# Kernel tuning notes

Hardware: AMD Instinct MI355X
Metric: run time of the kernel (lower is better)

The kernel has to match this reference:

```python
import jax, jax.numpy as jnp
import numpy as np

B, D, M = 64, 256, 100  # batch, reduced channel dim, h*w of feature map (10x10)

# Precompute upper-triangle (including diagonal) flat indices for Triuvec
_r, _c = np.triu_indices(D)
FLAT_TRIU_IDX = jnp.asarray(_r * D + _c)  # [D*(D+1)/2]


def setup_inputs() -> dict:
    key = jax.random.key(0)
    k1, = jax.random.split(key, 1)
    feat_map = jax.random.normal(k1, (B, D, M), dtype=jnp.float32)
    # temperature param init: log(1 / (2 * h * w)) with h = w = 10
    temperature = jnp.full((1, 1), np.log(1.0 / (2 * 10 * 10)), dtype=jnp.float32)
    return {"feat_map": feat_map, "temperature": temperature}


def reference(feat_map, temperature):
    # feat_map: [B, D, M]; temperature: [1, 1] learned scalar
    b, d, m = feat_map.shape
    f1 = feat_map[:, :, None, :]  # [B, D, 1, M]
    f2 = feat_map[:, None, :, :]  # [B, 1, D, M]
    # item_1 - item_2, summed over map dim; idea_variant path: (i1 - i2)/2 * exp(T)
    out = 0.5 * jnp.sum(jnp.abs(f1 + f2) - jnp.abs(f1 - f2), axis=-1)  # [B, D, D]
    out = out * jnp.exp(temperature[0, 0])
    # normalize_bdc double-centering: out - (1/D) out @ 1 - (1/D) 1 @ out
    row = jnp.sum(out, axis=2, keepdims=True) / d  # [B, D, 1]
    col = jnp.sum(out, axis=1, keepdims=True) / d  # [B, 1, D]
    out = out - row - col
    # Triuvec (with diagonal): gather upper-triangle entries
    vec = out.reshape(b, d * d)[:, FLAT_TRIU_IDX]  # [B, D*(D+1)/2]
    return vec
```

## Files before the change

### kernel.cpp

```cpp
#include <hip/hip_runtime.h>


#define NB 64
#define DD 256
#define MM 100
#define TILE 64
#define NUT 10
#define TRI_PER_B 32896
#define NTILE 640
#define NM2 50
#define TILE_F (TILE * TILE)
#define PSTRIDE 192

typedef unsigned int u32;
typedef _Float16 f16x2 __attribute__((ext_vector_type(2)));
typedef _Float16 f16x4 __attribute__((ext_vector_type(4)));

__device__ __forceinline__ void tile_coords(int t, int& ti, int& tj) {
    int a = (t >= 4) + (t >= 7) + (t >= 9);
    int s = (a * (9 - a)) >> 1;
    ti = a;
    tj = t - s + a;
}

__device__ __forceinline__ u32 slot_enc(int g) {
    return g == 0 ? 0x03020100u : g == 1 ? 0x21060504u
         : g == 2 ? 0x25220807u : 0x28262309u;
}

__device__ __forceinline__ int swz_bt(int w) { return (w & 7) * 80 + (w >> 3); }

extern "C" __global__ void __launch_bounds__(256, 5)
k_partial(const float* __restrict__ f, float* __restrict__ part,
          _Float16* __restrict__ tiles) {
    __shared__ u32 As[NM2][TILE];
    __shared__ u32 Bs[NM2][32];
    const int t = threadIdx.x;
    const int unit = (blockIdx.x & 7) * 160 + (blockIdx.x >> 3);
    const int bt = unit >> 1;
    const int half = unit & 1;
    const int b = bt / NUT;
    const int ut = bt % NUT;
    int ti, tj;
    tile_coords(ut, ti, tj);
    const int i0 = ti * TILE;
    const int j0 = tj * TILE + half * 32;
    const float* fb = f + (size_t)b * DD * MM;

    for (int l = t; l < TILE * 25; l += 256) {
        const int il = l & 63;
        const int mq = l >> 6;
        float4 v = *reinterpret_cast<const float4*>(fb + (size_t)(i0 + il) * MM + mq * 4);
        As[2 * mq + 0][il] = __builtin_bit_cast(u32, __builtin_amdgcn_cvt_pkrtz(v.x, v.y));
        As[2 * mq + 1][il] = __builtin_bit_cast(u32, __builtin_amdgcn_cvt_pkrtz(v.z, v.w));
    }
    for (int l = t; l < 32 * 25; l += 256) {
        const int il = l & 31;
        const int mq = l >> 5;
        float4 w = *reinterpret_cast<const float4*>(fb + (size_t)(j0 + il) * MM + mq * 4);
        Bs[2 * mq + 0][il] = __builtin_bit_cast(u32, __builtin_amdgcn_cvt_pkrtz(w.x, w.y));
        Bs[2 * mq + 1][il] = __builtin_bit_cast(u32, __builtin_amdgcn_cvt_pkrtz(w.z, w.w));
    }
    __syncthreads();

    const int cg = t & 15;
    const int rg = t >> 4;
    float acc[4][2] = {};

    uint4 af = *reinterpret_cast<const uint4*>(&As[0][rg * 4]);
    uint2 bf = *reinterpret_cast<const uint2*>(&Bs[0][cg * 2]);
    #pragma unroll 5
    for (int m2 = 0; m2 < NM2; ++m2) {
        uint4 an;
        uint2 bn;
        if (m2 + 1 < NM2) {
            an = *reinterpret_cast<const uint4*>(&As[m2 + 1][rg * 4]);
            bn = *reinterpret_cast<const uint2*>(&Bs[m2 + 1][cg * 2]);
        }
        const u32 av[4] = {af.x, af.y, af.z, af.w};
        const u32 bv[2] = {bf.x, bf.y};
        u32 aab[4], aso[4], bab[2], bsg[2];
        #pragma unroll
        for (int q = 0; q < 4; ++q) {
            aab[q] = av[q] & 0x7fff7fffu;
            aso[q] = (av[q] & 0x80008000u) | 0x3c003c00u;
        }
        #pragma unroll
        for (int c = 0; c < 2; ++c) {
            bab[c] = bv[c] & 0x7fff7fffu;
            bsg[c] = bv[c] & 0x80008000u;
        }
        #pragma unroll
        for (int q = 0; q < 4; ++q) {
            #pragma unroll
            for (int c = 0; c < 2; ++c) {
                u32 so = aso[q] ^ bsg[c];
                f16x2 mn = __builtin_elementwise_min(
                    __builtin_bit_cast(f16x2, aab[q]),
                    __builtin_bit_cast(f16x2, bab[c]));
                acc[q][c] = __builtin_amdgcn_fdot2(
                    mn, __builtin_bit_cast(f16x2, so), acc[q][c], false);
            }
        }
        af = an; bf = bn;
    }

    _Float16* tp = tiles + (size_t)bt * TILE_F;
    #pragma unroll
    for (int q = 0; q < 4; ++q) {
        *reinterpret_cast<u32*>(tp + (rg * 4 + q) * TILE + half * 32 + cg * 2) =
            __builtin_bit_cast(u32, __builtin_amdgcn_cvt_pkrtz(acc[q][0], acc[q][1]));
    }

    float ra[4], cb[2];
    #pragma unroll
    for (int q = 0; q < 4; ++q) ra[q] = acc[q][0] + acc[q][1];
    #pragma unroll
    for (int c = 0; c < 2; ++c)
        cb[c] = (acc[0][c] + acc[1][c]) + (acc[2][c] + acc[3][c]);

    __syncthreads();
    float* red  = reinterpret_cast<float*>(&As[0][0]);
    float* red2 = red + 1024;
    #pragma unroll
    for (int q = 0; q < 4; ++q) red[cg * 64 + rg * 4 + q] = ra[q];
    #pragma unroll
    for (int c = 0; c < 2; ++c) red2[rg * 32 + cg * 2 + c] = cb[c];
    __syncthreads();

    float* pb = part + (size_t)bt * PSTRIDE;
    if (t < TILE) {
        float s = 0.f;
        #pragma unroll
        for (int w = 0; w < 16; ++w) s += red[w * 64 + t];
        pb[half * 64 + t] = s;
    } else if (t < TILE + 32 && ti != tj) {
        const int u = t - TILE;
        float s = 0.f;
        #pragma unroll
        for (int w = 0; w < 16; ++w) s += red2[w * 32 + u];
        pb[128 + half * 32 + u] = s;
    }
}

extern "C" __global__ void __launch_bounds__(256)
k_finalize(const float* __restrict__ part, const float* __restrict__ temp,
           const _Float16* __restrict__ tiles, float* __restrict__ out) {
    __shared__ float rows_sh[128];
    const int t = threadIdx.x;
    const int bt = swz_bt(blockIdx.x);
    const int b = bt / NUT;
    const int ut = bt % NUT;
    int ti, tj;
    tile_coords(ut, ti, tj);
    const int i0 = ti * TILE, j0 = tj * TILE;
    const int tix = t >> 4, tiy = t & 15;

    if (t < 128) {
        const int hr = t >> 6, u = t & 63;
        const int g = hr ? tj : ti;
        const u32 enc = slot_enc(g);
        float sum = 0.f;
        #pragma unroll
        for (int s = 0; s < 4; ++s) {
            const u32 byte = (enc >> (8 * s)) & 0xffu;
            const int ut_s = byte & 0x1f;
            const int side = byte >> 5;
            const float* pb = part + (size_t)(b * NUT + ut_s) * PSTRIDE;
            sum += side ? pb[128 + u] : (pb[u] + pb[64 + u]);
        }
        rows_sh[t] = sum;
    }

    const _Float16* tp = tiles + (size_t)bt * TILE_F;
    float acc[4][4];
    #pragma unroll
    for (int q = 0; q < 4; ++q) {
        f16x4 v = *reinterpret_cast<const f16x4*>(tp + (tix * 4 + q) * TILE + tiy * 4);
        acc[q][0] = (float)v.x; acc[q][1] = (float)v.y;
        acc[q][2] = (float)v.z; acc[q][3] = (float)v.w;
    }
    __syncthreads();

    const float scale = expf(temp[0]);
    const float inv_d = 1.0f / DD;
    const int cbase = (ti == tj) ? 0 : 64;
    float rloc[4], cloc[4];
    #pragma unroll
    for (int q = 0; q < 4; ++q) rloc[q] = rows_sh[tix * 4 + q];
    #pragma unroll
    for (int r = 0; r < 4; ++r) cloc[r] = rows_sh[cbase + tiy * 4 + r];

    float* ob = out + (size_t)b * TRI_PER_B;
    #pragma unroll
    for (int q = 0; q < 4; ++q) {
        const int i = i0 + tix * 4 + q;
        float v[4];
        #pragma unroll
        for (int r = 0; r < 4; ++r)
            v[r] = scale * (acc[q][r] - (rloc[q] + cloc[r]) * inv_d);
        const int j0e = j0 + tiy * 4;
        if (ti != tj) {
            const int off = (i * (2 * DD - i + 1)) / 2 + (j0e - i);
            *reinterpret_cast<float4*>(ob + off) = make_float4(v[0], v[1], v[2], v[3]);
        } else {
            #pragma unroll
            for (int r = 0; r < 4; ++r) {
                const int j = j0e + r;
                if (j >= i) {
                    const int off = (i * (2 * DD - i + 1)) / 2 + (j - i);
                    ob[off] = v[r];
                }
            }
        }
    }
}

extern "C" void kernel_launch(void* const* d_in, const int* in_sizes, int n_in,
                              void* d_out, int out_size, void* d_ws, size_t ws_size,
                              hipStream_t stream) {
    const float* f    = (const float*)d_in[0];
    const float* temp = (const float*)d_in[1];
    float* out  = (float*)d_out;
    float* part = (float*)d_ws;
    _Float16* tiles = (_Float16*)(part + NTILE * PSTRIDE);

    k_partial<<<2 * NTILE, 256, 0, stream>>>(f, part, tiles);
    k_finalize<<<NTILE, 256, 0, stream>>>(part, temp, tiles, out);
}
```

Measured before the change: 36.17 us.

## Interleave m-pairs in LDS, stagger chunk order, split finalize into half-tiles

```diff
diff --git a/kernel.cpp b/kernel.cpp
--- a/kernel.cpp
+++ b/kernel.cpp
@@ -8,13 +8,12 @@
 #define NUT 10
 #define TRI_PER_B 32896
 #define NTILE 640
-#define NM2 50
+#define NMQ 25
 #define TILE_F (TILE * TILE)
 #define PSTRIDE 192
 
 typedef unsigned int u32;
 typedef _Float16 f16x2 __attribute__((ext_vector_type(2)));
-typedef _Float16 f16x4 __attribute__((ext_vector_type(4)));
 
 __device__ __forceinline__ void tile_coords(int t, int& ti, int& tj) {
     int a = (t >= 4) + (t >= 7) + (t >= 9);
@@ -28,13 +27,11 @@
          : g == 2 ? 0x25220807u : 0x28262309u;
 }
 
-__device__ __forceinline__ int swz_bt(int w) { return (w & 7) * 80 + (w >> 3); }
-
 extern "C" __global__ void __launch_bounds__(256, 5)
 k_partial(const float* __restrict__ f, float* __restrict__ part,
           _Float16* __restrict__ tiles) {
-    __shared__ u32 As[NM2][TILE];
-    __shared__ u32 Bs[NM2][32];
+    __shared__ u32 As[NMQ][TILE][2];
+    __shared__ u32 Bs[NMQ][32][2];
     const int t = threadIdx.x;
     const int unit = (blockIdx.x & 7) * 160 + (blockIdx.x >> 3);
     const int bt = unit >> 1;
@@ -47,19 +44,23 @@
     const int j0 = tj * TILE + half * 32;
     const float* fb = f + (size_t)b * DD * MM;
 
-    for (int l = t; l < TILE * 25; l += 256) {
+    for (int l = t; l < TILE * NMQ; l += 256) {
         const int il = l & 63;
         const int mq = l >> 6;
         float4 v = *reinterpret_cast<const float4*>(fb + (size_t)(i0 + il) * MM + mq * 4);
-        As[2 * mq + 0][il] = __builtin_bit_cast(u32, __builtin_amdgcn_cvt_pkrtz(v.x, v.y));
-        As[2 * mq + 1][il] = __builtin_bit_cast(u32, __builtin_amdgcn_cvt_pkrtz(v.z, v.w));
-    }
-    for (int l = t; l < 32 * 25; l += 256) {
+        uint2 p;
+        p.x = __builtin_bit_cast(u32, __builtin_amdgcn_cvt_pkrtz(v.x, v.y));
+        p.y = __builtin_bit_cast(u32, __builtin_amdgcn_cvt_pkrtz(v.z, v.w));
+        *reinterpret_cast<uint2*>(&As[mq][il][0]) = p;
+    }
+    for (int l = t; l < 32 * NMQ; l += 256) {
         const int il = l & 31;
         const int mq = l >> 5;
         float4 w = *reinterpret_cast<const float4*>(fb + (size_t)(j0 + il) * MM + mq * 4);
-        Bs[2 * mq + 0][il] = __builtin_bit_cast(u32, __builtin_amdgcn_cvt_pkrtz(w.x, w.y));
-        Bs[2 * mq + 1][il] = __builtin_bit_cast(u32, __builtin_amdgcn_cvt_pkrtz(w.z, w.w));
+        uint2 p;
+        p.x = __builtin_bit_cast(u32, __builtin_amdgcn_cvt_pkrtz(w.x, w.y));
+        p.y = __builtin_bit_cast(u32, __builtin_amdgcn_cvt_pkrtz(w.z, w.w));
+        *reinterpret_cast<uint2*>(&Bs[mq][il][0]) = p;
     }
     __syncthreads();
 
@@ -67,42 +68,49 @@
     const int rg = t >> 4;
     float acc[4][2] = {};
 
-    uint4 af = *reinterpret_cast<const uint4*>(&As[0][rg * 4]);
-    uint2 bf = *reinterpret_cast<const uint2*>(&Bs[0][cg * 2]);
-    #pragma unroll 5
-    for (int m2 = 0; m2 < NM2; ++m2) {
-        uint4 an;
-        uint2 bn;
-        if (m2 + 1 < NM2) {
-            an = *reinterpret_cast<const uint4*>(&As[m2 + 1][rg * 4]);
-            bn = *reinterpret_cast<const uint2*>(&Bs[m2 + 1][cg * 2]);
-        }
-        const u32 av[4] = {af.x, af.y, af.z, af.w};
-        const u32 bv[2] = {bf.x, bf.y};
-        u32 aab[4], aso[4], bab[2], bsg[2];
-        #pragma unroll
-        for (int q = 0; q < 4; ++q) {
-            aab[q] = av[q] & 0x7fff7fffu;
-            aso[q] = (av[q] & 0x80008000u) | 0x3c003c00u;
-        }
-        #pragma unroll
-        for (int c = 0; c < 2; ++c) {
-            bab[c] = bv[c] & 0x7fff7fffu;
-            bsg[c] = bv[c] & 0x80008000u;
-        }
-        #pragma unroll
-        for (int q = 0; q < 4; ++q) {
+    const int c0 = (int)(((t >> 6) + blockIdx.x) % 5u);
+    for (int cc = 0; cc < 5; ++cc) {
+        int ch = c0 + cc;
+        if (ch >= 5) ch -= 5;
+        const int mqb = ch * 5;
+        #pragma unroll
+        for (int k = 0; k < 5; ++k) {
+            const int mq = mqb + k;
+            uint4 alo = *reinterpret_cast<const uint4*>(&As[mq][rg * 4 + 0][0]);
+            uint4 ahi = *reinterpret_cast<const uint4*>(&As[mq][rg * 4 + 2][0]);
+            uint4 bb  = *reinterpret_cast<const uint4*>(&Bs[mq][cg * 2][0]);
+            const u32 al[4] = {alo.x, alo.y, alo.z, alo.w};
+            const u32 ah[4] = {ahi.x, ahi.y, ahi.z, ahi.w};
+            const u32 bl[4] = {bb.x, bb.y, bb.z, bb.w};
             #pragma unroll
-            for (int c = 0; c < 2; ++c) {
-                u32 so = aso[q] ^ bsg[c];
-                f16x2 mn = __builtin_elementwise_min(
-                    __builtin_bit_cast(f16x2, aab[q]),
-                    __builtin_bit_cast(f16x2, bab[c]));
-                acc[q][c] = __builtin_amdgcn_fdot2(
-                    mn, __builtin_bit_cast(f16x2, so), acc[q][c], false);
+            for (int e = 0; e < 2; ++e) {
+                const u32 av[4] = {al[e], al[2 + e], ah[e], ah[2 + e]};
+                const u32 bv[2] = {bl[e], bl[2 + e]};
+                u32 aab[4], aso[4], bab[2], bsg[2];
+                #pragma unroll
+                for (int q = 0; q < 4; ++q) {
+                    aab[q] = av[q] & 0x7fff7fffu;
+                    aso[q] = (av[q] & 0x80008000u) | 0x3c003c00u;
+                }
+                #pragma unroll
+                for (int c = 0; c < 2; ++c) {
+                    bab[c] = bv[c] & 0x7fff7fffu;
+                    bsg[c] = bv[c] & 0x80008000u;
+                }
+                #pragma unroll
+                for (int q = 0; q < 4; ++q) {
+                    #pragma unroll
+                    for (int c = 0; c < 2; ++c) {
+                        u32 so = aso[q] ^ bsg[c];
+                        f16x2 mn = __builtin_elementwise_min(
+                            __builtin_bit_cast(f16x2, aab[q]),
+                            __builtin_bit_cast(f16x2, bab[c]));
+                        acc[q][c] = __builtin_amdgcn_fdot2(
+                            mn, __builtin_bit_cast(f16x2, so), acc[q][c], false);
+                    }
+                }
             }
         }
-        af = an; bf = bn;
     }
 
     _Float16* tp = tiles + (size_t)bt * TILE_F;
@@ -120,7 +128,7 @@
         cb[c] = (acc[0][c] + acc[1][c]) + (acc[2][c] + acc[3][c]);
 
     __syncthreads();
-    float* red  = reinterpret_cast<float*>(&As[0][0]);
+    float* red  = reinterpret_cast<float*>(&As[0][0][0]);
     float* red2 = red + 1024;
     #pragma unroll
     for (int q = 0; q < 4; ++q) red[cg * 64 + rg * 4 + q] = ra[q];
@@ -148,17 +156,20 @@
            const _Float16* __restrict__ tiles, float* __restrict__ out) {
     __shared__ float rows_sh[128];
     const int t = threadIdx.x;
-    const int bt = swz_bt(blockIdx.x);
+    const int unit = (blockIdx.x & 7) * 160 + (blockIdx.x >> 3);
+    const int bt = unit >> 1;
+    const int half = unit & 1;
     const int b = bt / NUT;
     const int ut = bt % NUT;
     int ti, tj;
     tile_coords(ut, ti, tj);
-    const int i0 = ti * TILE, j0 = tj * TILE;
+    const int i0 = ti * TILE, j0 = tj * TILE + half * 32;
     const int tix = t >> 4, tiy = t & 15;
 
-    if (t < 128) {
-        const int hr = t >> 6, u = t & 63;
-        const int g = hr ? tj : ti;
+    if (t < 96) {
+        const int isrow = (t < 64);
+        const int u = isrow ? t : (half * 32 + (t - 64));
+        const int g = isrow ? ti : tj;
         const u32 enc = slot_enc(g);
         float sum = 0.f;
         #pragma unroll
@@ -173,45 +184,41 @@
     }
 
     const _Float16* tp = tiles + (size_t)bt * TILE_F;
-    float acc[4][4];
+    float vv[4][2];
     #pragma unroll
     for (int q = 0; q < 4; ++q) {
-        f16x4 v = *reinterpret_cast<const f16x4*>(tp + (tix * 4 + q) * TILE + tiy * 4);
-        acc[q][0] = (float)v.x; acc[q][1] = (float)v.y;
-        acc[q][2] = (float)v.z; acc[q][3] = (float)v.w;
+        u32 w = *reinterpret_cast<const u32*>(
+            tp + (tix * 4 + q) * TILE + half * 32 + tiy * 2);
+        f16x2 hv = __builtin_bit_cast(f16x2, w);
+        vv[q][0] = (float)hv.x;
+        vv[q][1] = (float)hv.y;
     }
     __syncthreads();
 
     const float scale = expf(temp[0]);
     const float inv_d = 1.0f / DD;
-    const int cbase = (ti == tj) ? 0 : 64;
-    float rloc[4], cloc[4];
+    float rloc[4], cloc[2];
     #pragma unroll
     for (int q = 0; q < 4; ++q) rloc[q] = rows_sh[tix * 4 + q];
     #pragma unroll
-    for (int r = 0; r < 4; ++r) cloc[r] = rows_sh[cbase + tiy * 4 + r];
+    for (int c = 0; c < 2; ++c) {
+        const int lc = tiy * 2 + c;
+        cloc[c] = (ti == tj) ? rows_sh[half * 32 + lc] : rows_sh[64 + lc];
+    }
 
     float* ob = out + (size_t)b * TRI_PER_B;
     #pragma unroll
     for (int q = 0; q < 4; ++q) {
         const int i = i0 + tix * 4 + q;
-        float v[4];
-        #pragma unroll
-        for (int r = 0; r < 4; ++r)
-            v[r] = scale * (acc[q][r] - (rloc[q] + cloc[r]) * inv_d);
-        const int j0e = j0 + tiy * 4;
+        const int j0e = j0 + tiy * 2;
+        float v0 = scale * (vv[q][0] - (rloc[q] + cloc[0]) * inv_d);
+        float v1 = scale * (vv[q][1] - (rloc[q] + cloc[1]) * inv_d);
         if (ti != tj) {
             const int off = (i * (2 * DD - i + 1)) / 2 + (j0e - i);
-            *reinterpret_cast<float4*>(ob + off) = make_float4(v[0], v[1], v[2], v[3]);
+            *reinterpret_cast<float2*>(ob + off) = make_float2(v0, v1);
         } else {
-            #pragma unroll
-            for (int r = 0; r < 4; ++r) {
-                const int j = j0e + r;
-                if (j >= i) {
-                    const int off = (i * (2 * DD - i + 1)) / 2 + (j - i);
-                    ob[off] = v[r];
-                }
-            }
+            if (j0e >= i)     ob[(i * (2 * DD - i + 1)) / 2 + (j0e - i)]     = v0;
+            if (j0e + 1 >= i) ob[(i * (2 * DD - i + 1)) / 2 + (j0e + 1 - i)] = v1;
         }
     }
 }
@@ -226,5 +233,5 @@
     _Float16* tiles = (_Float16*)(part + NTILE * PSTRIDE);
 
     k_partial<<<2 * NTILE, 256, 0, stream>>>(f, part, tiles);
-    k_finalize<<<NTILE, 256, 0, stream>>>(part, temp, tiles, out);
-}
+    k_finalize<<<2 * NTILE, 256, 0, stream>>>(part, temp, tiles, out);
+}
```

New measurement: 35.81 us. About the same (-1.0%).
